# Kernel optimization log

Hardware: AMD Instinct MI355X
Metric: run time of the kernel (lower is better)

The kernel has to match this reference:

```python
import jax, jax.numpy as jnp
import numpy as np

TEMPERATURE = 1.0  # SpriteAssembler.compositing_temperature
EPS = 1e-6


def setup_inputs() -> dict:
    key = jax.random.key(0)
    k1, k2 = jax.random.split(key)
    B, H, W, N = 8, 256, 256, 64
    shapes = jax.random.uniform(k1, (B, H, W, N), dtype=jnp.float32)  # occupancy in [0,1]
    depths = jax.random.normal(k2, (B, N), dtype=jnp.float32)
    return {"shapes": shapes, "depths": depths}


def reference(shapes, depths):
    # custom_composite: depth-ordered log-space alpha compositing.
    # mask_i = s_i * prod_j (1 - s_j) ** tanh(relu((d_j - d_i)/T)), then normalize.
    d = depths / max(TEMPERATURE, 1e-6)                      # [B, N]
    s = jnp.clip(shapes, EPS, 1.0 - EPS)                     # [B, H, W, N]
    # occlusion weights: w[b, i, j] = tanh(relu(d_j - d_i))
    w = jnp.tanh(jax.nn.relu(d[:, None, :] - d[:, :, None]))  # [B, N, N]
    log1m = jnp.log1p(-s)                                    # log(1 - s), [B, H, W, N]
    # log_mask_i = log(s_i) + sum_j log(1 - s_j) * w[i, j]  (j == i term is 0 since w[i,i]=0)
    log_masks = jnp.log(s) + jnp.einsum('bhwj,bij->bhwi', log1m, w)
    unnormalized = jnp.exp(log_masks)                        # [B, H, W, N]
    masks = unnormalized / (jnp.sum(unnormalized, axis=-1, keepdims=True) + EPS)
    return masks
```

## Files before the change

kernel.cpp:

```cpp
#include <hip/hip_runtime.h>


typedef __attribute__((ext_vector_type(8))) _Float16 half8;
typedef __attribute__((ext_vector_type(4))) float floatx4;

#define EPSF 1e-6f

__device__ inline float fast_exp2(float x){ return __builtin_amdgcn_exp2f(x); }
__device__ inline float fast_log2(float x){ return __builtin_amdgcn_logf(x); }
__device__ inline float fast_rcp (float x){ return __builtin_amdgcn_rcpf(x); }

__global__ __launch_bounds__(256, 2) void sprite_mfma_kernel(
    const float* __restrict__ shapes,
    const float* __restrict__ depths,
    float* __restrict__ out)
{
    const int wave  = threadIdx.x >> 6;
    const int lane  = threadIdx.x & 63;
    const int batch = blockIdx.x >> 7;
    const int rblk  = blockIdx.x & 127;
    const int wid   = rblk * 4 + wave;

    __shared__ float dsh[64];
    __shared__ __align__(16) float ustage[4][16][68];

    if (threadIdx.x < 64) dsh[threadIdx.x] = depths[batch * 64 + threadIdx.x];
    __syncthreads();

    const int c = lane & 15;
    const int q = lane >> 4;

    half8 Aw[4][2];
    #pragma unroll
    for (int it = 0; it < 4; ++it) {
        float di = dsh[it * 16 + c];
        #pragma unroll
        for (int kt = 0; kt < 2; ++kt) {
            half8 h;
            #pragma unroll
            for (int jj = 0; jj < 8; ++jj) {
                int j = kt * 32 + q * 8 + jj;
                float x = fmaxf(dsh[j] - di, 0.0f);
                float e = fast_exp2(x * 2.885390082f);
                h[jj] = (_Float16)((e - 1.0f) * fast_rcp(e + 1.0f));
            }
            Aw[it][kt] = h;
        }
    }

    half8 idlo, idhi;
    #pragma unroll
    for (int jj = 0; jj < 8; ++jj) {
        idlo[jj] = (q * 8 + jj == c)      ? (_Float16)1.0f : (_Float16)0.0f;
        idhi[jj] = (q * 8 + jj == 16 + c) ? (_Float16)1.0f : (_Float16)0.0f;
    }

    const long pxbase = (long)batch * 65536 + (long)wid * 128;
    const float* sp = shapes + (pxbase + c) * 64 + q * 8;
    float* const obase0 = out + pxbase * 64;

    float4 pf0 = *(const float4*)(sp);
    float4 pf1 = *(const float4*)(sp + 4);
    float4 pf2 = *(const float4*)(sp + 32);
    float4 pf3 = *(const float4*)(sp + 36);

    #pragma clang loop unroll(disable)
    for (int tile = 0; tile < 8; ++tile) {
        float4 s0 = pf0, s1 = pf1, s2 = pf2, s3 = pf3;
        {
            int tn = tile < 7 ? tile + 1 : 7;
            const float* sn = sp + tn * 16 * 64;
            pf0 = *(const float4*)(sn);
            pf1 = *(const float4*)(sn + 4);
            pf2 = *(const float4*)(sn + 32);
            pf3 = *(const float4*)(sn + 36);
        }

        float sv[16] = {s0.x, s0.y, s0.z, s0.w, s1.x, s1.y, s1.z, s1.w,
                        s2.x, s2.y, s2.z, s2.w, s3.x, s3.y, s3.z, s3.w};
        half8 B_lo, B_hi;
        half8 C_lo, C_hi;
        #pragma unroll
        for (int e = 0; e < 8; ++e) {
            float slo = fminf(fmaxf(sv[e],     EPSF), 1.0f - EPSF);
            float shi = fminf(fmaxf(sv[8 + e], EPSF), 1.0f - EPSF);
            B_lo[e] = (_Float16)fast_log2(1.0f - slo);
            B_hi[e] = (_Float16)fast_log2(1.0f - shi);
            C_lo[e] = (_Float16)fast_log2(slo);
            C_hi[e] = (_Float16)fast_log2(shi);
        }

        floatx4 acc[4];
        #pragma unroll
        for (int it = 0; it < 4; ++it) {
            floatx4 a = {0.f, 0.f, 0.f, 0.f};
            a = __builtin_amdgcn_mfma_f32_16x16x32_f16(Aw[it][0], B_lo, a, 0, 0, 0);
            a = __builtin_amdgcn_mfma_f32_16x16x32_f16(Aw[it][1], B_hi, a, 0, 0, 0);
            a = __builtin_amdgcn_mfma_f32_16x16x32_f16(
                    (it & 1) ? idhi : idlo, (it < 2) ? C_lo : C_hi, a, 0, 0, 0);
            acc[it] = a;
        }

        float u[4][4];
        float tot = 0.f;
        #pragma unroll
        for (int it = 0; it < 4; ++it) {
            #pragma unroll
            for (int r = 0; r < 4; ++r) {
                float v = fast_exp2(acc[it][r]);
                u[it][r] = v;
                tot += v;
            }
        }
        tot += __shfl_xor(tot, 16, 64);
        tot += __shfl_xor(tot, 32, 64);
        float inv = fast_rcp(tot + EPSF);

        #pragma unroll
        for (int it = 0; it < 4; ++it) {
            floatx4 o = {u[it][0] * inv, u[it][1] * inv,
                         u[it][2] * inv, u[it][3] * inv};
            *(floatx4*)&ustage[wave][c][it * 16 + q * 4] = o;
        }
        float* ob = obase0 + (long)tile * 16 * 64;
        #pragma unroll
        for (int k = 0; k < 4; ++k) {
            floatx4 o = *(const floatx4*)&ustage[wave][k * 4 + q][c * 4];
            *(floatx4*)(ob + k * 256 + lane * 4) = o;
        }
    }
}

extern "C" void kernel_launch(void* const* d_in, const int* in_sizes, int n_in,
                              void* d_out, int out_size, void* d_ws, size_t ws_size,
                              hipStream_t stream) {
    const float* shapes = (const float*)d_in[0];
    const float* depths = (const float*)d_in[1];
    float* out = (float*)d_out;
    sprite_mfma_kernel<<<1024, 256, 0, stream>>>(shapes, depths, out);
}
```

Measured before the change: 238.6 us.

## Precompute occlusion weights in a prep kernel and launch one tile per wave

Moves the tanh occlusion-weight computation into a separate small kernel that writes fp16 weights to workspace. The main kernel loads them instead of recomputing them per block. The main kernel also drops its 8-tile loop with software prefetch: each wave now handles a single 16-pixel tile, and the grid grows from 1024 to 8192 blocks. This relies on occupancy for latency hiding instead of explicit prefetch, and adds a second launch plus per-block weight loads from global memory.

```diff
diff --git a/kernel.cpp b/kernel.cpp
--- a/kernel.cpp
+++ b/kernel.cpp
@@ -10,42 +10,53 @@
 __device__ inline float fast_log2(float x){ return __builtin_amdgcn_logf(x); }
 __device__ inline float fast_rcp (float x){ return __builtin_amdgcn_rcpf(x); }
 
+__global__ __launch_bounds__(64) void w_prep_kernel(
+    const float* __restrict__ depths,
+    _Float16* __restrict__ w)
+{
+    const int b = blockIdx.x;
+    const int i = threadIdx.x;
+    __shared__ float dsh[64];
+    dsh[i] = depths[b * 64 + i];
+    __syncthreads();
+    const float di = dsh[i];
+    _Float16* wrow = w + (b * 64 + i) * 64;
+    #pragma unroll
+    for (int kt = 0; kt < 8; ++kt) {
+        half8 h;
+        #pragma unroll
+        for (int jj = 0; jj < 8; ++jj) {
+            float x = fmaxf(dsh[kt * 8 + jj] - di, 0.0f);
+            float e = fast_exp2(x * 2.885390082f);
+            h[jj] = (_Float16)((e - 1.0f) * fast_rcp(e + 1.0f));
+        }
+        *(half8*)(wrow + kt * 8) = h;
+    }
+}
+
 __global__ __launch_bounds__(256, 2) void sprite_mfma_kernel(
     const float* __restrict__ shapes,
-    const float* __restrict__ depths,
+    const _Float16* __restrict__ w,
     float* __restrict__ out)
 {
     const int wave  = threadIdx.x >> 6;
     const int lane  = threadIdx.x & 63;
-    const int batch = blockIdx.x >> 7;
-    const int rblk  = blockIdx.x & 127;
+    const int batch = blockIdx.x >> 10;
+    const int rblk  = blockIdx.x & 1023;
     const int wid   = rblk * 4 + wave;
 
-    __shared__ float dsh[64];
     __shared__ __align__(16) float ustage[4][16][68];
-
-    if (threadIdx.x < 64) dsh[threadIdx.x] = depths[batch * 64 + threadIdx.x];
-    __syncthreads();
 
     const int c = lane & 15;
     const int q = lane >> 4;
 
     half8 Aw[4][2];
+    const _Float16* wb = w + batch * 4096;
     #pragma unroll
     for (int it = 0; it < 4; ++it) {
-        float di = dsh[it * 16 + c];
         #pragma unroll
-        for (int kt = 0; kt < 2; ++kt) {
-            half8 h;
-            #pragma unroll
-            for (int jj = 0; jj < 8; ++jj) {
-                int j = kt * 32 + q * 8 + jj;
-                float x = fmaxf(dsh[j] - di, 0.0f);
-                float e = fast_exp2(x * 2.885390082f);
-                h[jj] = (_Float16)((e - 1.0f) * fast_rcp(e + 1.0f));
-            }
-            Aw[it][kt] = h;
-        }
+        for (int kt = 0; kt < 2; ++kt)
+            Aw[it][kt] = *(const half8*)(wb + (it * 16 + c) * 64 + kt * 32 + q * 8);
     }
 
     half8 idlo, idhi;
@@ -55,79 +66,64 @@
         idhi[jj] = (q * 8 + jj == 16 + c) ? (_Float16)1.0f : (_Float16)0.0f;
     }
 
-    const long pxbase = (long)batch * 65536 + (long)wid * 128;
-    const float* sp = shapes + (pxbase + c) * 64 + q * 8;
-    float* const obase0 = out + pxbase * 64;
+    const long px0 = (long)batch * 65536 + (long)wid * 16;
+    const float* sp = shapes + (px0 + c) * 64 + q * 8;
+    float4 s0 = *(const float4*)(sp);
+    float4 s1 = *(const float4*)(sp + 4);
+    float4 s2 = *(const float4*)(sp + 32);
+    float4 s3 = *(const float4*)(sp + 36);
 
-    float4 pf0 = *(const float4*)(sp);
-    float4 pf1 = *(const float4*)(sp + 4);
-    float4 pf2 = *(const float4*)(sp + 32);
-    float4 pf3 = *(const float4*)(sp + 36);
+    float sv[16] = {s0.x, s0.y, s0.z, s0.w, s1.x, s1.y, s1.z, s1.w,
+                    s2.x, s2.y, s2.z, s2.w, s3.x, s3.y, s3.z, s3.w};
+    half8 B_lo, B_hi;
+    half8 C_lo, C_hi;
+    #pragma unroll
+    for (int e = 0; e < 8; ++e) {
+        float slo = fminf(fmaxf(sv[e],     EPSF), 1.0f - EPSF);
+        float shi = fminf(fmaxf(sv[8 + e], EPSF), 1.0f - EPSF);
+        B_lo[e] = (_Float16)fast_log2(1.0f - slo);
+        B_hi[e] = (_Float16)fast_log2(1.0f - shi);
+        C_lo[e] = (_Float16)fast_log2(slo);
+        C_hi[e] = (_Float16)fast_log2(shi);
+    }
 
-    #pragma clang loop unroll(disable)
-    for (int tile = 0; tile < 8; ++tile) {
-        float4 s0 = pf0, s1 = pf1, s2 = pf2, s3 = pf3;
-        {
-            int tn = tile < 7 ? tile + 1 : 7;
-            const float* sn = sp + tn * 16 * 64;
-            pf0 = *(const float4*)(sn);
-            pf1 = *(const float4*)(sn + 4);
-            pf2 = *(const float4*)(sn + 32);
-            pf3 = *(const float4*)(sn + 36);
+    floatx4 acc[4];
+    #pragma unroll
+    for (int it = 0; it < 4; ++it) {
+        floatx4 a = {0.f, 0.f, 0.f, 0.f};
+        a = __builtin_amdgcn_mfma_f32_16x16x32_f16(Aw[it][0], B_lo, a, 0, 0, 0);
+        a = __builtin_amdgcn_mfma_f32_16x16x32_f16(Aw[it][1], B_hi, a, 0, 0, 0);
+        a = __builtin_amdgcn_mfma_f32_16x16x32_f16(
+                (it & 1) ? idhi : idlo, (it < 2) ? C_lo : C_hi, a, 0, 0, 0);
+        acc[it] = a;
+    }
+
+    float u[4][4];
+    float tot = 0.f;
+    #pragma unroll
+    for (int it = 0; it < 4; ++it) {
+        #pragma unroll
+        for (int r = 0; r < 4; ++r) {
+            float v = fast_exp2(acc[it][r]);
+            u[it][r] = v;
+            tot += v;
         }
+    }
+    tot += __shfl_xor(tot, 16, 64);
+    tot += __shfl_xor(tot, 32, 64);
+    float inv = fast_rcp(tot + EPSF);
 
-        float sv[16] = {s0.x, s0.y, s0.z, s0.w, s1.x, s1.y, s1.z, s1.w,
-                        s2.x, s2.y, s2.z, s2.w, s3.x, s3.y, s3.z, s3.w};
-        half8 B_lo, B_hi;
-        half8 C_lo, C_hi;
-        #pragma unroll
-        for (int e = 0; e < 8; ++e) {
-            float slo = fminf(fmaxf(sv[e],     EPSF), 1.0f - EPSF);
-            float shi = fminf(fmaxf(sv[8 + e], EPSF), 1.0f - EPSF);
-            B_lo[e] = (_Float16)fast_log2(1.0f - slo);
-            B_hi[e] = (_Float16)fast_log2(1.0f - shi);
-            C_lo[e] = (_Float16)fast_log2(slo);
-            C_hi[e] = (_Float16)fast_log2(shi);
-        }
-
-        floatx4 acc[4];
-        #pragma unroll
-        for (int it = 0; it < 4; ++it) {
-            floatx4 a = {0.f, 0.f, 0.f, 0.f};
-            a = __builtin_amdgcn_mfma_f32_16x16x32_f16(Aw[it][0], B_lo, a, 0, 0, 0);
-            a = __builtin_amdgcn_mfma_f32_16x16x32_f16(Aw[it][1], B_hi, a, 0, 0, 0);
-            a = __builtin_amdgcn_mfma_f32_16x16x32_f16(
-                    (it & 1) ? idhi : idlo, (it < 2) ? C_lo : C_hi, a, 0, 0, 0);
-            acc[it] = a;
-        }
-
-        float u[4][4];
-        float tot = 0.f;
-        #pragma unroll
-        for (int it = 0; it < 4; ++it) {
-            #pragma unroll
-            for (int r = 0; r < 4; ++r) {
-                float v = fast_exp2(acc[it][r]);
-                u[it][r] = v;
-                tot += v;
-            }
-        }
-        tot += __shfl_xor(tot, 16, 64);
-        tot += __shfl_xor(tot, 32, 64);
-        float inv = fast_rcp(tot + EPSF);
-
-        #pragma unroll
-        for (int it = 0; it < 4; ++it) {
-            floatx4 o = {u[it][0] * inv, u[it][1] * inv,
-                         u[it][2] * inv, u[it][3] * inv};
-            *(floatx4*)&ustage[wave][c][it * 16 + q * 4] = o;
-        }
-        float* ob = obase0 + (long)tile * 16 * 64;
-        #pragma unroll
-        for (int k = 0; k < 4; ++k) {
-            floatx4 o = *(const floatx4*)&ustage[wave][k * 4 + q][c * 4];
-            *(floatx4*)(ob + k * 256 + lane * 4) = o;
-        }
+    #pragma unroll
+    for (int it = 0; it < 4; ++it) {
+        floatx4 o = {u[it][0] * inv, u[it][1] * inv,
+                     u[it][2] * inv, u[it][3] * inv};
+        *(floatx4*)&ustage[wave][c][it * 16 + q * 4] = o;
+    }
+    float* ob = out + px0 * 64;
+    #pragma unroll
+    for (int k = 0; k < 4; ++k) {
+        floatx4 o = *(const floatx4*)&ustage[wave][k * 4 + q][c * 4];
+        *(floatx4*)(ob + k * 256 + lane * 4) = o;
     }
 }
 
@@ -137,5 +133,7 @@
     const float* shapes = (const float*)d_in[0];
     const float* depths = (const float*)d_in[1];
     float* out = (float*)d_out;
-    sprite_mfma_kernel<<<1024, 256, 0, stream>>>(shapes, depths, out);
+    _Float16* w = (_Float16*)d_ws;
+    w_prep_kernel<<<8, 64, 0, stream>>>(depths, w);
+    sprite_mfma_kernel<<<8192, 256, 0, stream>>>(shapes, w, out);
 }
```

Measured after the change: 233.0 us. 1.02x faster.
